# Optimization experiments

Measured on AMD Instinct MI355X. Metric: run time of the kernel, lower is better.

## Reference

```python
import jax, jax.numpy as jnp
import numpy as np

N_STATE = 64
H_DIM = 128
CHANNELS = 1
SEQ_LEN = 8192
EPS = 1e-7
DT_MIN, DT_MAX = 1e-3, 1e-1


def setup_inputs() -> dict:
    key = jax.random.key(0)
    k1, k2 = jax.random.split(key)
    # Lambda ~ hippo_skew_pos_imag init: real part -0.5, imag parts ~ skew-hippo evals
    # (stored as real pairs [N,2], matching _c2r(Lambda))
    lam_re = -0.5 * jnp.ones((N_STATE,), jnp.float32)
    lam_im = jnp.pi * jnp.arange(N_STATE, dtype=jnp.float32)
    Lambda = jnp.stack([lam_re, lam_im], axis=-1)                      # [N,2]
    # log_dt uniform in [log dt_min, log dt_max], tiled for separate re/im dt
    u = jax.random.uniform(k1, (H_DIM,), jnp.float32)
    log_dt_1 = np.log(DT_MIN) + u * (np.log(DT_MAX) - np.log(DT_MIN))  # [H]
    log_dt = jnp.tile(log_dt_1[:, None], (1, 2))                       # [H,2]
    W = jax.random.normal(k2, (CHANNELS, H_DIM, N_STATE, 2), jnp.float32)
    return {"L": SEQ_LEN, "Lambda": Lambda, "log_dt": log_dt, "W": W}


def reference(L, Lambda, log_dt, W):
    """DSS 'softmax' kernel (arxiv 2203.14343). Returns real kernel K [C,H,L]."""
    Lam = Lambda[:, 0] + 1j * Lambda[:, 1]                             # [N] complex64
    dt = jnp.exp(log_dt)                                               # [H,2]
    # separate dt for real and imag parts (sep_dt_re_im=True)
    dt_Lambda = dt[:, 0:1] * Lam.real + 1j * dt[:, 1:2] * Lam.imag     # [H,N]

    pos = jnp.arange(L, dtype=jnp.float32)                             # [L]
    gt0 = Lam.real > 0                                                 # [N]
    # stabilizing shift for Re(Lambda)>0 modes (detached, as in torch.no_grad)
    P_max = jax.lax.stop_gradient(dt_Lambda * jnp.where(gt0, jnp.float32(L - 1), 0.0))
    P = dt_Lambda[..., None] * pos - P_max[..., None]                  # [H,N,L]
    S = jnp.exp(P)                                                     # [H,N,L] complex Vandermonde

    # structured-softmax normalization: W *= (e^{dtL}-1) / ((e^{L dtL}-1) * Lambda)
    dtL_neg = dt_Lambda * jnp.where(gt0, -1.0, 1.0)                    # [H,N]
    num = jnp.exp(dtL_neg) - 1.0                                       # [H,N]
    den = jnp.exp(jnp.float32(L) * dtL_neg) - 1.0                      # [H,N]
    x = den * Lam                                                      # [H,N]
    recip = jnp.conj(x) / ((x * jnp.conj(x)).real + EPS)               # bounded 1/x
    Wc = (W[..., 0] + 1j * W[..., 1]) * num * recip                    # [C,H,N]

    K = jnp.einsum('chn,hnl->chl', Wc, S)                              # [C,H,L]
    return K.real.astype(jnp.float32)                                  # kernel_to_real='real'
```

## Files before the change

kernel.cpp:

```cpp
#include <hip/hip_runtime.h>
#include <math.h>


#if __has_builtin(__builtin_amdgcn_sinf)
__device__ inline float vsin_rev(float x) { return __builtin_amdgcn_sinf(x); }
__device__ inline float vcos_rev(float x) { return __builtin_amdgcn_cosf(x); }
#else
__device__ inline float vsin_rev(float x) { return __sinf(x * 6.28318530717958647692f); }
__device__ inline float vcos_rev(float x) { return __cosf(x * 6.28318530717958647692f); }
#endif

typedef float v2f __attribute__((ext_vector_type(2)));

#define KPT 8
#define TPB 256

__global__ __launch_bounds__(TPB) void dss_kernel(
    const float* __restrict__ Lambda,
    const float* __restrict__ log_dt,
    const float* __restrict__ W,
    float* __restrict__ out,
    int H, int N, int L, int C, int chunks)
{
    __shared__ float4 pA[64];
    __shared__ float4 pB[64];
    __shared__ float2 pC[64];

    const int h     = blockIdx.x / chunks;
    const int chunk = blockIdx.x % chunks;
    const int c     = blockIdx.y;
    const int tid   = threadIdx.x;

    if (tid < N) {
        const int n = tid;
        double dt0 = exp((double)log_dt[h*2 + 0]);
        double dt1 = exp((double)log_dt[h*2 + 1]);
        double lre = (double)Lambda[n*2 + 0];
        double lim = (double)Lambda[n*2 + 1];
        double zr = dt0 * lre;
        double zi = dt1 * lim;
        bool gt0 = (lre > 0.0);
        double sgn = gt0 ? -1.0 : 1.0;
        double dnr = sgn * zr, dni = sgn * zi;
        double ednr  = exp(dnr);
        double num_re = ednr * cos(dni) - 1.0;
        double num_im = ednr * sin(dni);
        double Ld = (double)L;
        double eLr = exp(Ld * dnr);
        double den_re = eLr * cos(Ld * dni) - 1.0;
        double den_im = eLr * sin(Ld * dni);
        double x_re = den_re * lre - den_im * lim;
        double x_im = den_re * lim + den_im * lre;
        double inv  = 1.0 / (x_re*x_re + x_im*x_im + 1e-7);
        double r_re =  x_re * inv;
        double r_im = -x_im * inv;
        double m_re = num_re * r_re - num_im * r_im;
        double m_im = num_re * r_im + num_im * r_re;
        double w0 = (double)W[((size_t)(c*H + h)*N + n)*2 + 0];
        double w1 = (double)W[((size_t)(c*H + h)*N + n)*2 + 1];
        double wr = w0 * m_re - w1 * m_im;
        double wi = w0 * m_im + w1 * m_re;
        double loff = gt0 ? (double)(L - 1) : 0.0;

        const double LOG2E  = 1.4426950408889634074;
        const double INV2PI = 0.15915494309189533577;
        double er = zr * LOG2E;
        double ph = zi * INV2PI;
        float ph_hi = (float)ph;
        float ph_lo = (float)(ph - (double)ph_hi);

        double Sd  = (double)TPB;
        double mag = exp(zr * Sd);
        double ang = zi * Sd;
        double Rr  = mag * cos(ang);
        double Ri  = mag * sin(ang);
        double c1  = 2.0 * Rr;
        double c2  = -(mag * mag);

        pA[n] = make_float4((float)wr, (float)wi, (float)er, (float)loff);
        pB[n] = make_float4(ph_hi, ph_lo, (float)c1, (float)c2);
        pC[n] = make_float2((float)Rr, (float)Ri);
    }
    __syncthreads();

    const int lchunk = KPT * TPB;
    const int lbase  = chunk * lchunk;
    const float x0f  = (float)(lbase + tid);

    v2f acc2a[KPT], acc2b[KPT];
    #pragma unroll
    for (int k = 0; k < KPT; ++k) { acc2a[k] = (v2f)(0.0f); acc2b[k] = (v2f)(0.0f); }

    for (int n = 0; n < N; n += 4) {
        float4 A[4], B[4]; float2 Rv[4];
        #pragma unroll
        for (int j = 0; j < 4; ++j) { A[j] = pA[n+j]; B[j] = pB[n+j]; Rv[j] = pC[n+j]; }

        float X0[4], X1[4];
        #pragma unroll
        for (int j = 0; j < 4; ++j) {
            const float4 a = A[j]; const float4 b = B[j]; const float2 r = Rv[j];
            float x  = x0f - a.w;
            float e  = __builtin_amdgcn_exp2f(a.z * x);
            float p  = b.x * x;
            float e1 = fmaf(b.x, x, -p);
            float f  = (p - floorf(p)) + fmaf(b.y, x, e1);
            float s  = vsin_rev(f);
            float co = vcos_rev(f);
            float tr = fmaf(a.x, co, -(a.y * s));
            float ti = fmaf(a.x, s,   a.y * co);
            float Tr = e * tr;
            float Ti = e * ti;
            X0[j] = Tr;
            X1[j] = fmaf(Tr, r.x, -(Ti * r.y));
        }

        v2f x0a = {X0[0], X0[1]}, x1a = {X1[0], X1[1]};
        v2f x0b = {X0[2], X0[3]}, x1b = {X1[2], X1[3]};
        v2f c1a = {B[0].z, B[1].z}, c2a = {B[0].w, B[1].w};
        v2f c1b = {B[2].z, B[3].z}, c2b = {B[2].w, B[3].w};

        acc2a[0] += x0a; acc2a[1] += x1a;
        acc2b[0] += x0b; acc2b[1] += x1b;
        #pragma unroll
        for (int k = 2; k < KPT; ++k) {
            v2f ta = c2a * x0a;
            v2f xa = __builtin_elementwise_fma(c1a, x1a, ta);
            acc2a[k] += xa; x0a = x1a; x1a = xa;
            v2f tb = c2b * x0b;
            v2f xb = __builtin_elementwise_fma(c1b, x1b, tb);
            acc2b[k] += xb; x0b = x1b; x1b = xb;
        }
    }

    float* o = out + ((size_t)c * H + h) * (size_t)L + lbase + tid;
    #pragma unroll
    for (int k = 0; k < KPT; ++k) {
        int l = lbase + tid + k * TPB;
        if (l < L) o[k * TPB] = acc2a[k].x + acc2a[k].y + acc2b[k].x + acc2b[k].y;
    }
}

extern "C" void kernel_launch(void* const* d_in, const int* in_sizes, int n_in,
                              void* d_out, int out_size, void* d_ws, size_t ws_size,
                              hipStream_t stream) {
    const float* Lambda = (const float*)d_in[1];
    const float* log_dt = (const float*)d_in[2];
    const float* W      = (const float*)d_in[3];
    float* out = (float*)d_out;

    const int N = in_sizes[1] / 2;
    const int H = in_sizes[2] / 2;
    const int C = in_sizes[3] / (2 * H * N);
    const int L = out_size / (C * H);

    const int per_block = KPT * TPB;
    const int chunks = (L + per_block - 1) / per_block;
    dim3 grid(H * chunks, C);
    dss_kernel<<<grid, TPB, 0, stream>>>(Lambda, log_dt, W, out, H, N, L, C, chunks);
}
```

Measured before the change: 17.17 us.

## Precompute per-mode coefficients in prep kernel and split state sum across thread groups

Moves the double-precision per-(h,n) coefficient computation into a separate prep kernel writing to workspace, so main blocks no longer redundantly recompute it per chunk. The main kernel now uses 512 threads per block, splitting the N-state loop between two groups and combining partial sums through shared memory. This aims to remove serialized fp64 setup and raise occupancy, at the cost of an extra kernel launch, a workspace round trip, and an additional barrier.

```diff
diff --git a/kernel.cpp b/kernel.cpp
--- a/kernel.cpp
+++ b/kernel.cpp
@@ -12,94 +12,117 @@
 
 typedef float v2f __attribute__((ext_vector_type(2)));
 
-#define KPT 8
-#define TPB 256
-
-__global__ __launch_bounds__(TPB) void dss_kernel(
+#define KPT   8
+#define TPB_L 256
+#define NSPLIT 2
+#define TPB   (TPB_L * NSPLIT)
+
+__global__ __launch_bounds__(256) void dss_prep(
     const float* __restrict__ Lambda,
     const float* __restrict__ log_dt,
     const float* __restrict__ W,
+    float4* __restrict__ ws,
+    int H, int N, int L, int C)
+{
+    int idx = blockIdx.x * blockDim.x + threadIdx.x;
+    int total = C * H * N;
+    if (idx >= total) return;
+    int n = idx % N;
+    int hc = idx / N;
+    int h = hc % H;
+
+    double dt0 = exp((double)log_dt[h*2 + 0]);
+    double dt1 = exp((double)log_dt[h*2 + 1]);
+    double lre = (double)Lambda[n*2 + 0];
+    double lim = (double)Lambda[n*2 + 1];
+    double zr = dt0 * lre;
+    double zi = dt1 * lim;
+    bool gt0 = (lre > 0.0);
+    double sgn = gt0 ? -1.0 : 1.0;
+    double dnr = sgn * zr, dni = sgn * zi;
+    double ednr  = exp(dnr);
+    double num_re = ednr * cos(dni) - 1.0;
+    double num_im = ednr * sin(dni);
+    double Ld = (double)L;
+    double eLr = exp(Ld * dnr);
+    double den_re = eLr * cos(Ld * dni) - 1.0;
+    double den_im = eLr * sin(Ld * dni);
+    double x_re = den_re * lre - den_im * lim;
+    double x_im = den_re * lim + den_im * lre;
+    double inv  = 1.0 / (x_re*x_re + x_im*x_im + 1e-7);
+    double r_re =  x_re * inv;
+    double r_im = -x_im * inv;
+    double m_re = num_re * r_re - num_im * r_im;
+    double m_im = num_re * r_im + num_im * r_re;
+    double w0 = (double)W[(size_t)idx*2 + 0];
+    double w1 = (double)W[(size_t)idx*2 + 1];
+    double wr = w0 * m_re - w1 * m_im;
+    double wi = w0 * m_im + w1 * m_re;
+    double loff = gt0 ? (double)(L - 1) : 0.0;
+
+    const double LOG2E  = 1.4426950408889634074;
+    const double INV2PI = 0.15915494309189533577;
+    double er = zr * LOG2E;
+    double ph = zi * INV2PI;
+    float ph_hi = (float)ph;
+    float ph_lo = (float)(ph - (double)ph_hi);
+
+    double Sd  = (double)TPB_L;
+    double mag = exp(zr * Sd);
+    double ang = zi * Sd;
+    double Rr  = mag * cos(ang);
+    double Ri  = mag * sin(ang);
+    double c1  = 2.0 * Rr;
+    double c2  = -(mag * mag);
+
+    float4* base = ws + (size_t)hc * 3 * N;
+    base[0*N + n] = make_float4((float)wr, (float)wi, (float)er, (float)loff);
+    base[1*N + n] = make_float4(ph_hi, ph_lo, (float)c1, (float)c2);
+    base[2*N + n] = make_float4((float)Rr, (float)Ri, 0.0f, 0.0f);
+}
+
+__global__ __launch_bounds__(TPB) void dss_main(
+    const float4* __restrict__ ws,
     float* __restrict__ out,
     int H, int N, int L, int C, int chunks)
 {
-    __shared__ float4 pA[64];
-    __shared__ float4 pB[64];
-    __shared__ float2 pC[64];
+    __shared__ float4 sP[3 * 64];
+    __shared__ float  comb[KPT][TPB_L];
 
     const int h     = blockIdx.x / chunks;
     const int chunk = blockIdx.x % chunks;
     const int c     = blockIdx.y;
     const int tid   = threadIdx.x;
-
-    if (tid < N) {
-        const int n = tid;
-        double dt0 = exp((double)log_dt[h*2 + 0]);
-        double dt1 = exp((double)log_dt[h*2 + 1]);
-        double lre = (double)Lambda[n*2 + 0];
-        double lim = (double)Lambda[n*2 + 1];
-        double zr = dt0 * lre;
-        double zi = dt1 * lim;
-        bool gt0 = (lre > 0.0);
-        double sgn = gt0 ? -1.0 : 1.0;
-        double dnr = sgn * zr, dni = sgn * zi;
-        double ednr  = exp(dnr);
-        double num_re = ednr * cos(dni) - 1.0;
-        double num_im = ednr * sin(dni);
-        double Ld = (double)L;
-        double eLr = exp(Ld * dnr);
-        double den_re = eLr * cos(Ld * dni) - 1.0;
-        double den_im = eLr * sin(Ld * dni);
-        double x_re = den_re * lre - den_im * lim;
-        double x_im = den_re * lim + den_im * lre;
-        double inv  = 1.0 / (x_re*x_re + x_im*x_im + 1e-7);
-        double r_re =  x_re * inv;
-        double r_im = -x_im * inv;
-        double m_re = num_re * r_re - num_im * r_im;
-        double m_im = num_re * r_im + num_im * r_re;
-        double w0 = (double)W[((size_t)(c*H + h)*N + n)*2 + 0];
-        double w1 = (double)W[((size_t)(c*H + h)*N + n)*2 + 1];
-        double wr = w0 * m_re - w1 * m_im;
-        double wi = w0 * m_im + w1 * m_re;
-        double loff = gt0 ? (double)(L - 1) : 0.0;
-
-        const double LOG2E  = 1.4426950408889634074;
-        const double INV2PI = 0.15915494309189533577;
-        double er = zr * LOG2E;
-        double ph = zi * INV2PI;
-        float ph_hi = (float)ph;
-        float ph_lo = (float)(ph - (double)ph_hi);
-
-        double Sd  = (double)TPB;
-        double mag = exp(zr * Sd);
-        double ang = zi * Sd;
-        double Rr  = mag * cos(ang);
-        double Ri  = mag * sin(ang);
-        double c1  = 2.0 * Rr;
-        double c2  = -(mag * mag);
-
-        pA[n] = make_float4((float)wr, (float)wi, (float)er, (float)loff);
-        pB[n] = make_float4(ph_hi, ph_lo, (float)c1, (float)c2);
-        pC[n] = make_float2((float)Rr, (float)Ri);
-    }
+    const int lt    = tid & (TPB_L - 1);
+    const int g     = tid >> 8;
+
+    if (tid < 3 * N) sP[tid] = ws[(size_t)(c*H + h) * 3 * N + tid];
     __syncthreads();
 
-    const int lchunk = KPT * TPB;
+    const float4* pA = sP;
+    const float4* pB = sP + N;
+    const float4* pC = sP + 2 * N;
+
+    const int lchunk = KPT * TPB_L;
     const int lbase  = chunk * lchunk;
-    const float x0f  = (float)(lbase + tid);
+    const float x0f  = (float)(lbase + lt);
 
     v2f acc2a[KPT], acc2b[KPT];
     #pragma unroll
     for (int k = 0; k < KPT; ++k) { acc2a[k] = (v2f)(0.0f); acc2b[k] = (v2f)(0.0f); }
 
-    for (int n = 0; n < N; n += 4) {
-        float4 A[4], B[4]; float2 Rv[4];
+    const int nbeg = g * (N / NSPLIT);
+    const int nend = nbeg + (N / NSPLIT);
+
+    for (int n = nbeg; n < nend; n += 4) {
+        float4 A[4], B[4], Rv[4];
         #pragma unroll
         for (int j = 0; j < 4; ++j) { A[j] = pA[n+j]; B[j] = pB[n+j]; Rv[j] = pC[n+j]; }
 
         float X0[4], X1[4];
         #pragma unroll
         for (int j = 0; j < 4; ++j) {
-            const float4 a = A[j]; const float4 b = B[j]; const float2 r = Rv[j];
+            const float4 a = A[j]; const float4 b = B[j]; const float4 r = Rv[j];
             float x  = x0f - a.w;
             float e  = __builtin_amdgcn_exp2f(a.z * x);
             float p  = b.x * x;
@@ -133,11 +156,23 @@
         }
     }
 
-    float* o = out + ((size_t)c * H + h) * (size_t)L + lbase + tid;
+    float tot[KPT];
     #pragma unroll
-    for (int k = 0; k < KPT; ++k) {
-        int l = lbase + tid + k * TPB;
-        if (l < L) o[k * TPB] = acc2a[k].x + acc2a[k].y + acc2b[k].x + acc2b[k].y;
+    for (int k = 0; k < KPT; ++k)
+        tot[k] = (acc2a[k].x + acc2a[k].y) + (acc2b[k].x + acc2b[k].y);
+
+    if (g == 1) {
+        #pragma unroll
+        for (int k = 0; k < KPT; ++k) comb[k][lt] = tot[k];
+    }
+    __syncthreads();
+    if (g == 0) {
+        float* o = out + ((size_t)c * H + h) * (size_t)L + lbase + lt;
+        #pragma unroll
+        for (int k = 0; k < KPT; ++k) {
+            int l = lbase + lt + k * TPB_L;
+            if (l < L) o[k * TPB_L] = tot[k] + comb[k][lt];
+        }
     }
 }
 
@@ -154,8 +189,13 @@
     const int C = in_sizes[3] / (2 * H * N);
     const int L = out_size / (C * H);
 
-    const int per_block = KPT * TPB;
+    float4* ws = (float4*)d_ws;
+
+    const int total = C * H * N;
+    dss_prep<<<(total + 255) / 256, 256, 0, stream>>>(Lambda, log_dt, W, ws, H, N, L, C);
+
+    const int per_block = KPT * TPB_L;
     const int chunks = (L + per_block - 1) / per_block;
     dim3 grid(H * chunks, C);
-    dss_kernel<<<grid, TPB, 0, stream>>>(Lambda, log_dt, W, out, H, N, L, C, chunks);
+    dss_main<<<grid, TPB, 0, stream>>>(ws, out, H, N, L, C, chunks);
 }
```

Result: slower. 20.91 us (+21.8%).

## Split state dimension across two thread groups and combine through shared memory

Applied to the files above, without the earlier changes.

Each block now has 512 threads. Two groups each handle half of the N state modes for the same 256 positions. Their partial sums are added through a shared-memory buffer before group 0 writes the output. The grid size is unchanged at 128x4=512 blocks, so the goal is more waves per CU and better latency hiding on a grid too small to fill the device. The cost is an extra __syncthreads, a shared-memory reduction, and half the threads sitting idle during the store.

```diff
diff --git a/kernel.cpp b/kernel.cpp
--- a/kernel.cpp
+++ b/kernel.cpp
@@ -12,8 +12,10 @@
 
 typedef float v2f __attribute__((ext_vector_type(2)));
 
-#define KPT 8
-#define TPB 256
+#define KPT    8
+#define TPB_L  256
+#define NSPLIT 2
+#define TPB    (TPB_L * NSPLIT)
 
 __global__ __launch_bounds__(TPB) void dss_kernel(
     const float* __restrict__ Lambda,
@@ -25,11 +27,14 @@
     __shared__ float4 pA[64];
     __shared__ float4 pB[64];
     __shared__ float2 pC[64];
+    __shared__ float  comb[KPT][TPB_L];
 
     const int h     = blockIdx.x / chunks;
     const int chunk = blockIdx.x % chunks;
     const int c     = blockIdx.y;
     const int tid   = threadIdx.x;
+    const int lt    = tid & (TPB_L - 1);
+    const int g     = tid >> 8;
 
     if (tid < N) {
         const int n = tid;
@@ -69,7 +74,7 @@
         float ph_hi = (float)ph;
         float ph_lo = (float)(ph - (double)ph_hi);
 
-        double Sd  = (double)TPB;
+        double Sd  = (double)TPB_L;
         double mag = exp(zr * Sd);
         double ang = zi * Sd;
         double Rr  = mag * cos(ang);
@@ -83,15 +88,18 @@
     }
     __syncthreads();
 
-    const int lchunk = KPT * TPB;
+    const int lchunk = KPT * TPB_L;
     const int lbase  = chunk * lchunk;
-    const float x0f  = (float)(lbase + tid);
+    const float x0f  = (float)(lbase + lt);
 
     v2f acc2a[KPT], acc2b[KPT];
     #pragma unroll
     for (int k = 0; k < KPT; ++k) { acc2a[k] = (v2f)(0.0f); acc2b[k] = (v2f)(0.0f); }
 
-    for (int n = 0; n < N; n += 4) {
+    const int nbeg = g * (N / NSPLIT);
+    const int nend = nbeg + (N / NSPLIT);
+
+    for (int n = nbeg; n < nend; n += 4) {
         float4 A[4], B[4]; float2 Rv[4];
         #pragma unroll
         for (int j = 0; j < 4; ++j) { A[j] = pA[n+j]; B[j] = pB[n+j]; Rv[j] = pC[n+j]; }
@@ -133,11 +141,23 @@
         }
     }
 
-    float* o = out + ((size_t)c * H + h) * (size_t)L + lbase + tid;
+    float tot[KPT];
     #pragma unroll
-    for (int k = 0; k < KPT; ++k) {
-        int l = lbase + tid + k * TPB;
-        if (l < L) o[k * TPB] = acc2a[k].x + acc2a[k].y + acc2b[k].x + acc2b[k].y;
+    for (int k = 0; k < KPT; ++k)
+        tot[k] = (acc2a[k].x + acc2a[k].y) + (acc2b[k].x + acc2b[k].y);
+
+    if (g == 1) {
+        #pragma unroll
+        for (int k = 0; k < KPT; ++k) comb[k][lt] = tot[k];
+    }
+    __syncthreads();
+    if (g == 0) {
+        float* o = out + ((size_t)c * H + h) * (size_t)L + lbase + lt;
+        #pragma unroll
+        for (int k = 0; k < KPT; ++k) {
+            int l = lbase + lt + k * TPB_L;
+            if (l < L) o[k * TPB_L] = tot[k] + comb[k][lt];
+        }
     }
 }
 
@@ -154,7 +174,7 @@
     const int C = in_sizes[3] / (2 * H * N);
     const int L = out_size / (C * H);
 
-    const int per_block = KPT * TPB;
+    const int per_block = KPT * TPB_L;
     const int chunks = (L + per_block - 1) / per_block;
     dim3 grid(H * chunks, C);
     dss_kernel<<<grid, TPB, 0, stream>>>(Lambda, log_dt, W, out, H, N, L, C, chunks);
```

Result: no change. 16.94 us (-1.4%).
